# Kernel optimization log

Hardware: AMD Instinct MI355X
Metric: run time of the kernel (lower is better)

Reference implementation:

```python
import jax, jax.numpy as jnp
import numpy as np

N = 10000        # nodes
F_IN = 128       # node features (data.num_node_features)
OUT = 16         # out_channels
H = 32           # attention heads
C1 = 4 * OUT     # hidden per-head dim (4*out_channels)
E = 80000        # directed edges
EPS = 1e-5       # BatchNorm eps
NEG = 0.2        # GATConv LeakyReLU negative_slope


def _gat(x, src, dst, W, a_s, a_d, b, n, C):
    # PyG GATConv, shared lin, concat=False (mean over heads)
    h = (x @ W).reshape(n, H, C)                    # [n,H,C]
    e_src = jnp.sum(h * a_s, -1)                    # [n,H] (alpha from x_j)
    e_dst = jnp.sum(h * a_d, -1)                    # [n,H] (alpha from x_i)
    e = jax.nn.leaky_relu(e_src[src] + e_dst[dst], NEG)     # [E',H]
    m = jax.ops.segment_max(e, dst, num_segments=n)         # segment softmax
    p = jnp.exp(e - m[dst])
    z = jax.ops.segment_sum(p, dst, num_segments=n)
    alpha = p / z[dst]
    out = jax.ops.segment_sum(alpha[:, :, None] * h[src], dst, num_segments=n)
    return out.mean(1) + b                          # mean over heads + bias


def _bn(x, g, b, m, v):  # eval-mode BatchNorm1d (running stats)
    return (x - m) * g / jnp.sqrt(v + EPS) + b


def setup_inputs():
    k = jax.random.split(jax.random.key(0), 40)
    rn = lambda i, s, sc=0.1: jax.random.normal(k[i], s, jnp.float32) * sc
    d = {"x": jax.random.normal(k[0], (N, F_IN), jnp.float32),
         "edge_index": jax.random.randint(k[1], (2, E), 0, N, jnp.int32)}
    # 4 GATConv layers
    d.update(W1=rn(2, (F_IN, H * C1)), as1=rn(3, (H, C1)), ad1=rn(4, (H, C1)), b1=rn(5, (C1,)))
    d.update(W2=rn(6, (C1, H * OUT)), as2=rn(7, (H, OUT)), ad2=rn(8, (H, OUT)), b2=rn(9, (OUT,)))
    d.update(W3=rn(10, (F_IN, H * C1)), as3=rn(11, (H, C1)), ad3=rn(12, (H, C1)), b3=rn(13, (C1,)))
    d.update(W4=rn(14, (C1, H * OUT)), as4=rn(15, (H, OUT)), ad4=rn(16, (H, OUT)), b4=rn(17, (OUT,)))
    # ResidualNetwork(1 block): 1x1 Conv1d over L=1 == matmul
    d.update(rwa=rn(18, (F_IN, OUT)), rba=rn(19, (OUT,)),
             bn1g=jnp.ones(OUT), bn1b=jnp.zeros(OUT), bn1m=rn(20, (OUT,)), bn1v=jnp.abs(rn(21, (OUT,))) + 1.0,
             rwb=rn(22, (OUT, OUT)), rbb=rn(23, (OUT,)),
             bn2g=jnp.ones(OUT), bn2b=jnp.zeros(OUT), bn2m=rn(24, (OUT,)), bn2v=jnp.abs(rn(25, (OUT,))) + 1.0,
             wsc=rn(26, (F_IN, OUT)), bsc=rn(27, (OUT,)),
             bnsg=jnp.ones(OUT), bnsb=jnp.zeros(OUT), bnsm=rn(28, (OUT,)), bnsv=jnp.abs(rn(29, (OUT,))) + 1.0,
             wfc=rn(30, (OUT, OUT)), bfc=rn(31, (OUT,)))
    return d


def reference(x, edge_index, W1, as1, ad1, b1, W2, as2, ad2, b2,
              W3, as3, ad3, b3, W4, as4, ad4, b4,
              rwa, rba, bn1g, bn1b, bn1m, bn1v, rwb, rbb, bn2g, bn2b, bn2m, bn2v,
              wsc, bsc, bnsg, bnsb, bnsm, bnsv, wfc, bfc):
    n = x.shape[0]
    loops = jnp.arange(n, dtype=edge_index.dtype)  # add_self_loops=True
    s2t_src = jnp.concatenate([edge_index[0], loops])  # flow source_to_target
    s2t_dst = jnp.concatenate([edge_index[1], loops])
    t2s_src = jnp.concatenate([edge_index[1], loops])  # flow target_to_source
    t2s_dst = jnp.concatenate([edge_index[0], loops])
    # dropout in original is unassigned (no-op); eval mode assumed
    x_s = jax.nn.elu(_gat(x, s2t_src, s2t_dst, W1, as1, ad1, b1, n, C1))
    x_in = jax.nn.elu(_gat(x_s, s2t_src, s2t_dst, W2, as2, ad2, b2, n, OUT))
    x_t = jax.nn.elu(_gat(x, t2s_src, t2s_dst, W3, as3, ad3, b3, n, C1))
    x_out = jax.nn.elu(_gat(x_t, t2s_src, t2s_dst, W4, as4, ad4, b4, n, OUT))
    # ResidualNetwork: block + identity avg-pool (L=1) + fc
    h = jax.nn.relu(_bn(x @ rwa + rba, bn1g, bn1b, bn1m, bn1v))
    h = _bn(h @ rwb + rbb, bn2g, bn2b, bn2m, bn2v)
    sc = _bn(x @ wsc + bsc, bnsg, bnsb, bnsm, bnsv)
    x_self = jax.nn.relu(h + sc) @ wfc + bfc
    return (x_in, x_out, x_self)
```

## Files before the change

### kernel.cpp

```cpp
#include <hip/hip_runtime.h>
#include <stdint.h>

__device__ __forceinline__ float bf2f(unsigned short u) {
  union { unsigned int i; float f; } v; v.i = ((unsigned int)u) << 16; return v.f;
}
__device__ __forceinline__ unsigned short f2bf(float f) {
  union { float f; unsigned int i; } v; v.f = f;
  unsigned int i = v.i;
  unsigned int r = (i + 0x7fffu + ((i >> 16) & 1u)) >> 16;
  return (unsigned short)r;
}

typedef __bf16 bf16x8 __attribute__((ext_vector_type(8)));
typedef float f32x4 __attribute__((ext_vector_type(4)));
typedef float f32x2 __attribute__((ext_vector_type(2)));
union ABfrag { int4 i4; bf16x8 v; };

#if __has_builtin(__builtin_amdgcn_cvt_pk_fp8_f32) && __has_builtin(__builtin_amdgcn_cvt_pk_f32_fp8)
#define HW_FP8 1
#else
#define HW_FP8 0
#endif

__device__ __forceinline__ unsigned char f2fp8_sw(float f) {
  union { float f; unsigned int u; } v; v.f = f;
  unsigned int s = (v.u >> 24) & 0x80;
  float a = fabsf(f);
  if (a >= 448.f) return (unsigned char)(s | 0x7E);
  v.f = a;
  int ex = (int)(v.u >> 23);
  unsigned int man = v.u & 0x7FFFFFu;
  if (ex >= 121) {
    unsigned int val = ((unsigned int)(ex - 120) << 3) | (man >> 20);
    unsigned int rem = man & 0xFFFFFu;
    if (rem > 0x80000u || (rem == 0x80000u && (val & 1))) val++;
    if (val > 0x7E) val = 0x7E;
    return (unsigned char)(s | val);
  }
  int q = (int)(a * 512.f + 0.5f);
  if (q > 8) q = 8;
  return (unsigned char)(s | (unsigned int)q);
}
__device__ __forceinline__ float fp8dec_sw(unsigned char c) {
  unsigned int e = (c >> 3) & 15u, m = c & 7u;
  float v;
  if (e) { union { unsigned int u; float f; } x; x.u = ((e + 120) << 23) | (m << 20); v = x.f; }
  else v = (float)m * 0.001953125f;
  return (c & 0x80) ? -v : v;
}
__device__ __forceinline__ unsigned char f2fp8(float f) {
#if HW_FP8
  int v = __builtin_amdgcn_cvt_pk_fp8_f32(f, f, 0, false);
  return (unsigned char)(v & 0xFF);
#else
  return f2fp8_sw(f);
#endif
}
__device__ __forceinline__ void dec16p(int4 g, f32x2 o[8]) {
#if HW_FP8
  o[0] = __builtin_amdgcn_cvt_pk_f32_fp8(g.x, false);
  o[1] = __builtin_amdgcn_cvt_pk_f32_fp8(g.x, true);
  o[2] = __builtin_amdgcn_cvt_pk_f32_fp8(g.y, false);
  o[3] = __builtin_amdgcn_cvt_pk_f32_fp8(g.y, true);
  o[4] = __builtin_amdgcn_cvt_pk_f32_fp8(g.z, false);
  o[5] = __builtin_amdgcn_cvt_pk_f32_fp8(g.z, true);
  o[6] = __builtin_amdgcn_cvt_pk_f32_fp8(g.w, false);
  o[7] = __builtin_amdgcn_cvt_pk_f32_fp8(g.w, true);
#else
  unsigned int w[4] = {(unsigned)g.x, (unsigned)g.y, (unsigned)g.z, (unsigned)g.w};
#pragma unroll
  for (int d = 0; d < 4; ++d) {
    unsigned int x = w[d];
    o[d * 2 + 0] = (f32x2){fp8dec_sw((unsigned char)(x & 0xFF)),
                           fp8dec_sw((unsigned char)((x >> 8) & 0xFF))};
    o[d * 2 + 1] = (f32x2){fp8dec_sw((unsigned char)((x >> 16) & 0xFF)),
                           fp8dec_sw((unsigned char)((x >> 24) & 0xFF))};
  }
#endif
}

__device__ __forceinline__ float lrelu_clamp(float e) {
  e = (e > 0.f) ? e : 0.2f * e;
  return fminf(e, 80.f);
}

__global__ __launch_bounds__(256) void k_detect(const unsigned int* __restrict__ x, int* flag,
                                                int* __restrict__ degAB, int ndeg2) {
  if (blockIdx.x == 0) {
    __shared__ int cnt;
    if (threadIdx.x == 0) cnt = 0;
    __syncthreads();
    int c = 0;
    for (int i = threadIdx.x; i < 1024; i += 256) {
      unsigned int lo = x[i] & 0xFFFFu;
      int ex = (int)((lo >> 7) & 0xFF);
      if (ex >= 100 && ex <= 140) c++;
    }
    atomicAdd(&cnt, c);
    __syncthreads();
    if (threadIdx.x == 0) flag[0] = (cnt > 600) ? 1 : 0;
    return;
  }
  for (int idx = (blockIdx.x - 1) * 256 + threadIdx.x; idx < ndeg2; idx += 8 * 256) degAB[idx] = 0;
}

struct PrepDesc {
  const void* csrc[32]; float* cdst[32]; int cn[32];
  const void* x; float* xc; unsigned short* xp;
  const void* W1; const void* W2; const void* W3; const void* W4;
  unsigned short* P1; unsigned short* P2; unsigned short* P3; unsigned short* P4;
  int* degAB;
  const int* ei;
  int nxb, xtotal, ctotal, E, nn;
};
__global__ __launch_bounds__(256) void k_prep(PrepDesc d, const int* __restrict__ flag) {
  int isbf = *flag;
  int b = blockIdx.x;
  if (b < d.nxb) {
    int i = b * 256 + threadIdx.x;
    if (i < d.xtotal) {
      float v = isbf ? bf2f(((const unsigned short*)d.x)[i]) : ((const float*)d.x)[i];
      d.xc[i] = v;
      int row = i >> 7, c = i & 127;
      int tm = row >> 4, mr = row & 15;
      int s = c >> 5, quad = (c >> 3) & 3, j = c & 7;
      size_t idx = (((size_t)tm * 4 + s) * 64 + quad * 16 + mr) * 8 + j;
      d.xp[idx] = f2bf(v);
    }
    return;
  }
  b -= d.nxb;
  if (b < 288) {
    int u = b * 256 + threadIdx.x;
    const void* W; unsigned short* P; int K, N, lu;
    if (u < 32768)      { W = d.W1; P = d.P1; K = 128; N = 2048; lu = u; }
    else if (u < 36864) { W = d.W2; P = d.P2; K = 64;  N = 512;  lu = u - 32768; }
    else if (u < 69632) { W = d.W3; P = d.P3; K = 128; N = 2048; lu = u - 36864; }
    else                { W = d.W4; P = d.P4; K = 64;  N = 512;  lu = u - 69632; }
    int ksteps = K >> 5;
    int g = lu / (ksteps * 64);
    int rem = lu - g * (ksteps * 64);
    int s = rem >> 6, lane = rem & 63;
    int mr = lane & 15, quad = lane >> 4;
    int col = g * 16 + mr;
    int kbase = s * 32 + quad * 8;
#pragma unroll
    for (int j = 0; j < 8; ++j) {
      size_t src = (size_t)(kbase + j) * N + col;
      float v = isbf ? bf2f(((const unsigned short*)W)[src]) : ((const float*)W)[src];
      P[(size_t)lu * 8 + j] = f2bf(v);
    }
    return;
  }
  b -= 288;
  if (b < 4) {
    for (int idx = b * 256 + threadIdx.x; idx < d.ctotal; idx += 4 * 256) {
      int t = 0, off = idx;
      while (off >= d.cn[t]) { off -= d.cn[t]; ++t; }
      float v = isbf ? bf2f(((const unsigned short*)d.csrc[t])[off])
                     : ((const float*)d.csrc[t])[off];
      d.cdst[t][off] = v;
    }
    return;
  }
  b -= 4;
  {
    int e = b * 256 + threadIdx.x;
    if (e < d.E) {
      atomicAdd(&d.degAB[d.ei[d.E + e]], 1);
      atomicAdd(&d.degAB[d.nn + d.ei[e]], 1);
    }
  }
}

__global__ __launch_bounds__(1024) void k_exscan2(const int* __restrict__ degA, const int* __restrict__ degB,
                                                  int* __restrict__ rowA, int* __restrict__ rowB,
                                                  int* __restrict__ colA, int* __restrict__ colB,
                                                  int* __restrict__ curA, int* __restrict__ curB, int n) {
  const int* deg = (blockIdx.x == 0) ? degA : degB;
  int* row = (blockIdx.x == 0) ? rowA : rowB;
  int* colx = (blockIdx.x == 0) ? colA : colB;
  int* curx = (blockIdx.x == 0) ? curA : curB;
  __shared__ int wsum[16], wbase[16];
  __shared__ int carry;
  if (threadIdx.x == 0) carry = 0;
  __syncthreads();
  int lane = threadIdx.x & 63, w = threadIdx.x >> 6;
  int chunks = (n + 1023) >> 10;
  for (int ch = 0; ch < chunks; ++ch) {
    int i = (ch << 10) + threadIdx.x;
    int v = (i < n) ? deg[i] : 0;
    int sc = v;
#pragma unroll
    for (int o = 1; o < 64; o <<= 1) { int t = __shfl_up(sc, o); if (lane >= o) sc += t; }
    if (lane == 63) wsum[w] = sc;
    __syncthreads();
    if (threadIdx.x < 16) {
      int v2 = wsum[threadIdx.x], s2 = v2;
#pragma unroll
      for (int o = 1; o < 16; o <<= 1) { int t = __shfl_up(s2, o); if (lane >= o) s2 += t; }
      wbase[threadIdx.x] = s2 - v2;
      if (threadIdx.x == 15) wsum[15] = s2;
    }
    __syncthreads();
    if (i < n) {
      int rv = carry + wbase[w] + (sc - v) + i;
      row[i] = rv;
      colx[rv] = i;
      curx[i] = rv + 1;
    }
    __syncthreads();
    if (threadIdx.x == 0) carry += wsum[15];
    __syncthreads();
  }
  if (threadIdx.x == 0) row[n] = carry + n;
}

union SMem {
  unsigned char tile[4][16][64];
  struct { float xs[16][128]; float ha[16][16]; float tt[16][16]; } res;
};

template<int CH, int KSTEPS>
__device__ __forceinline__ void mm_es_body(int vblk,
    const unsigned short* __restrict__ Ap, const unsigned short* __restrict__ Bp,
    unsigned char* __restrict__ C, const float* __restrict__ a_s, const float* __restrict__ a_d,
    float* __restrict__ es, float* __restrict__ ed, int N, SMem* sm) {
  int wid = threadIdx.x >> 6;
  int wg = vblk * 4 + wid;
  int ntiles = N >> 6;
  int tm = wg / ntiles, tn = wg % ntiles;
  int lane = threadIdx.x & 63;
  int mr = lane & 15, quad = lane >> 4;
  const unsigned short* ap = Ap + ((size_t)tm * KSTEPS) * 512 + lane * 8;
  const unsigned short* bp = Bp + ((size_t)tn * 4 * KSTEPS) * 512 + lane * 8;
  f32x4 acc[4];
#pragma unroll
  for (int i = 0; i < 4; i++) acc[i] = (f32x4){0.f, 0.f, 0.f, 0.f};
#pragma unroll
  for (int s = 0; s < KSTEPS; ++s) {
    ABfrag a; a.i4 = *(const int4*)(ap + s * 512);
#pragma unroll
    for (int nt = 0; nt < 4; ++nt) {
      ABfrag b; b.i4 = *(const int4*)(bp + (size_t)(nt * KSTEPS + s) * 512);
      acc[nt] = __builtin_amdgcn_mfma_f32_16x16x32_bf16(a.v, b.v, acc[nt], 0, 0, 0);
    }
  }
#pragma unroll
  for (int nt = 0; nt < 4; ++nt)
#pragma unroll
    for (int r = 0; r < 4; ++r)
      sm->tile[wid][quad * 4 + r][nt * 16 + mr] = f2fp8(acc[nt][r]);
  __syncthreads();
  {
    int r16 = lane >> 2, seg = lane & 3;
    int4 val = *(const int4*)&sm->tile[wid][r16][seg * 16];
    *(int4*)(C + (size_t)(tm * 16 + r16) * N + tn * 64 + seg * 16) = val;
  }
  if (CH == 64) {
    float pes[4] = {0.f,0.f,0.f,0.f}, ped[4] = {0.f,0.f,0.f,0.f};
    const float* asr = a_s + tn * 64;
    const float* adr = a_d + tn * 64;
#pragma unroll
    for (int nt = 0; nt < 4; ++nt) {
      float ws = asr[nt * 16 + mr], wd = adr[nt * 16 + mr];
#pragma unroll
      for (int r = 0; r < 4; ++r) { pes[r] += acc[nt][r] * ws; ped[r] += acc[nt][r] * wd; }
    }
#pragma unroll
    for (int m = 1; m < 16; m <<= 1)
#pragma unroll
      for (int r = 0; r < 4; ++r) {
        pes[r] += __shfl_xor(pes[r], m);
        ped[r] += __shfl_xor(ped[r], m);
      }
    if (mr == 0) {
#pragma unroll
      for (int r = 0; r < 4; ++r) {
        int row = tm * 16 + quad * 4 + r;
        es[row * 32 + tn] = pes[r];
        ed[row * 32 + tn] = ped[r];
      }
    }
  } else {
    float pes[4][4], ped[4][4];
#pragma unroll
    for (int nt = 0; nt < 4; ++nt) {
      float ws = a_s[(tn * 4 + nt) * 16 + mr];
      float wd = a_d[(tn * 4 + nt) * 16 + mr];
#pragma unroll
      for (int r = 0; r < 4; ++r) { pes[nt][r] = acc[nt][r] * ws; ped[nt][r] = acc[nt][r] * wd; }
    }
#pragma unroll
    for (int m = 1; m < 16; m <<= 1)
#pragma unroll
      for (int nt = 0; nt < 4; ++nt)
#pragma unroll
        for (int r = 0; r < 4; ++r) {
          pes[nt][r] += __shfl_xor(pes[nt][r], m);
          ped[nt][r] += __shfl_xor(ped[nt][r], m);
        }
    if (mr == 0) {
#pragma unroll
      for (int nt = 0; nt < 4; ++nt)
#pragma unroll
        for (int r = 0; r < 4; ++r) {
          int row = tm * 16 + quad * 4 + r;
          es[row * 32 + tn * 4 + nt] = pes[nt][r];
          ed[row * 32 + tn * 4 + nt] = ped[nt][r];
        }
    }
  }
}

struct MM13Desc {
  const unsigned short* Ap;
  const unsigned short* B1; const unsigned short* B3;
  unsigned char* C1; unsigned char* C3;
  const float* as1; const float* ad1; const float* as3; const float* ad3;
  float* es1; float* ed1; float* es3; float* ed3;
  int sblks, mmblks, resblks, E;
  const int* ei; int* colA; int* colB; int* curA; int* curB;
  const float* xc;
  const float* rp[20];
  void* outbase; size_t eoff; int n;
  const int* flag;
};
__global__ __launch_bounds__(256) void k_mm13res(MM13Desc d) {
  __shared__ SMem sm;
  int b = blockIdx.x;
  if (b < d.sblks) {
    int e = b * 256 + threadIdx.x;
    if (e < d.E) {
      int s = d.ei[e], dd = d.ei[d.E + e];
      d.colA[atomicAdd(&d.curA[dd], 1)] = s;
      d.colB[atomicAdd(&d.curB[s], 1)] = dd;
    }
    return;
  }
  b -= d.sblks;
  if (b < d.mmblks) {
    mm_es_body<64,4>(b, d.Ap, d.B1, d.C1, d.as1, d.ad1, d.es1, d.ed1, 2048, &sm);
    return;
  }
  b -= d.mmblks;
  if (b < d.mmblks) {
    mm_es_body<64,4>(b, d.Ap, d.B3, d.C3, d.as3, d.ad3, d.es3, d.ed3, 2048, &sm);
    return;
  }
  b -= d.mmblks;
  int nodebase = b * 16;
  for (int t = threadIdx.x; t < 16 * 128; t += 256)
    sm.res.xs[t >> 7][t & 127] = d.xc[(size_t)(nodebase + (t >> 7)) * 128 + (t & 127)];
  __syncthreads();
  int ni = threadIdx.x >> 4, c = threadIdx.x & 15;
  const float* rwa = d.rp[0]; const float* rba = d.rp[1];
  const float* bn1g = d.rp[2]; const float* bn1b = d.rp[3];
  const float* bn1m = d.rp[4]; const float* bn1v = d.rp[5];
  const float* rwb = d.rp[6]; const float* rbb = d.rp[7];
  const float* bn2g = d.rp[8]; const float* bn2b = d.rp[9];
  const float* bn2m = d.rp[10]; const float* bn2v = d.rp[11];
  const float* wsc = d.rp[12]; const float* bsc = d.rp[13];
  const float* bnsg = d.rp[14]; const float* bnsb = d.rp[15];
  const float* bnsm = d.rp[16]; const float* bnsv = d.rp[17];
  const float* wfc = d.rp[18]; const float* bfc = d.rp[19];
  float ya = 0.f, ysc = 0.f;
  for (int k = 0; k < 128; ++k) {
    float xv = sm.res.xs[ni][k];
    ya  += xv * rwa[k * 16 + c];
    ysc += xv * wsc[k * 16 + c];
  }
  ya += rba[c]; ysc += bsc[c];
  float s1 = bn1g[c] * rsqrtf(bn1v[c] + 1e-5f);
  ya = (ya - bn1m[c]) * s1 + bn1b[c];
  ya = fmaxf(ya, 0.f);
  float ss = bnsg[c] * rsqrtf(bnsv[c] + 1e-5f);
  ysc = (ysc - bnsm[c]) * ss + bnsb[c];
  sm.res.ha[ni][c] = ya;
  __syncthreads();
  float h2 = rbb[c];
  for (int k = 0; k < 16; ++k) h2 += sm.res.ha[ni][k] * rwb[k * 16 + c];
  float s2 = bn2g[c] * rsqrtf(bn2v[c] + 1e-5f);
  h2 = (h2 - bn2m[c]) * s2 + bn2b[c];
  sm.res.tt[ni][c] = fmaxf(h2 + ysc, 0.f);
  __syncthreads();
  float o = bfc[c];
  for (int k = 0; k < 16; ++k) o += sm.res.tt[ni][k] * wfc[k * 16 + c];
  size_t oo = d.eoff + (size_t)(nodebase + ni) * 16 + c;
  if (*d.flag) ((unsigned short*)d.outbase)[oo] = f2bf(o);
  else         ((float*)d.outbase)[oo] = o;
}

__global__ __launch_bounds__(256) void k_g64(const unsigned char* __restrict__ h1,
                                             const unsigned char* __restrict__ h3,
                                             const float* __restrict__ es1, const float* __restrict__ ed1,
                                             const float* __restrict__ es3, const float* __restrict__ ed3,
                                             const int* __restrict__ rowA, const int* __restrict__ colA,
                                             const int* __restrict__ rowB, const int* __restrict__ colB,
                                             const float* __restrict__ b1, const float* __restrict__ b3,
                                             unsigned short* __restrict__ xsp, unsigned short* __restrict__ xtp,
                                             int n, int gb) {
  int b = blockIdx.x;
  const unsigned char* h; const float *es, *ed, *bias; const int *rowp, *col; unsigned short* outp;
  if (b < gb) { h = h1; es = es1; ed = ed1; rowp = rowA; col = colA; bias = b1; outp = xsp; }
  else { b -= gb; h = h3; es = es3; ed = ed3; rowp = rowB; col = colB; bias = b3; outp = xtp; }
  int wid = threadIdx.x >> 6, lane = threadIdx.x & 63;
  int i = b * 4 + wid;
  if (i >= n) return;
  int hd0 = lane >> 2, hd1 = 16 + hd0;
  float e0 = ed[i * 32 + hd0];
  float e1 = ed[i * 32 + hd1];
  int beg = rowp[i], end = rowp[i + 1];
  int deg = end - beg;
  int colv = (lane < deg) ? col[beg + lane] : 0;
  f32x2 acc0[8], acc1[8];
#pragma unroll
  for (int k = 0; k < 8; ++k) { acc0[k] = (f32x2){0.f, 0.f}; acc1[k] = (f32x2){0.f, 0.f}; }
  float Z0 = 0.f, Z1 = 0.f;
  int s0 = __shfl(colv, 0);
  const int4* hp0 = (const int4*)(h + (size_t)s0 * 2048);
  int4 ng0 = hp0[lane];
  int4 ng1 = hp0[64 + lane];
  float na = es[s0 * 32 + hd0];
  float nb = es[s0 * 32 + hd1];
  for (int j = 0; j < deg; ++j) {
    int4 g0 = ng0, g1 = ng1;
    float ea = na, eb = nb;
    int jn = j + 1;
    if (jn < deg) {
      int sn = (jn < 64) ? __shfl(colv, jn) : col[beg + jn];
      const int4* hq = (const int4*)(h + (size_t)sn * 2048);
      ng0 = hq[lane];
      ng1 = hq[64 + lane];
      na = es[sn * 32 + hd0];
      nb = es[sn * 32 + hd1];
    }
    float q0 = __expf(lrelu_clamp(ea + e0));
    float q1 = __expf(lrelu_clamp(eb + e1));
    Z0 += q0; Z1 += q1;
    f32x2 d0[8], d1[8];
    dec16p(g0, d0); dec16p(g1, d1);
    f32x2 q0v = (f32x2){q0, q0}, q1v = (f32x2){q1, q1};
#pragma unroll
    for (int k = 0; k < 8; ++k) {
      acc0[k] = __builtin_elementwise_fma(q0v, d0[k], acc0[k]);
      acc1[k] = __builtin_elementwise_fma(q1v, d1[k], acc1[k]);
    }
  }
  float zi0 = 1.0f / Z0, zi1 = 1.0f / Z1;
  f32x2 zi0v = (f32x2){zi0, zi0}, zi1v = (f32x2){zi1, zi1};
  f32x2 v2[8];
#pragma unroll
  for (int k = 0; k < 8; ++k)
    v2[k] = __builtin_elementwise_fma(acc1[k], zi1v, acc0[k] * zi0v);
#pragma unroll
  for (int m = 4; m < 64; m <<= 1)
#pragma unroll
    for (int k = 0; k < 8; ++k) {
      v2[k].x += __shfl_xor(v2[k].x, m);
      v2[k].y += __shfl_xor(v2[k].y, m);
    }
  if (lane < 4) {
    float v[16];
#pragma unroll
    for (int k = 0; k < 8; ++k) { v[2 * k] = v2[k].x; v[2 * k + 1] = v2[k].y; }
    int tm = i >> 4, mr = i & 15;
    unsigned short ob[16];
#pragma unroll
    for (int k = 0; k < 16; ++k) {
      float t = v[k] * (1.f / 32.f) + bias[lane * 16 + k];
      t = (t > 0.f) ? t : (__expf(t) - 1.f);
      ob[k] = f2bf(t);
    }
    int s0w = lane >> 1;
#pragma unroll
    for (int g2 = 0; g2 < 2; ++g2) {
      size_t idx = (((size_t)tm * 2 + s0w) * 64 + ((lane & 1) * 2 + g2) * 16 + mr) * 8;
      *(int4*)(outp + idx) = *(const int4*)(ob + g2 * 8);
    }
  }
}

__global__ __launch_bounds__(256) void k_mm24(const unsigned short* __restrict__ xsp,
                                              const unsigned short* __restrict__ xtp,
                                              const unsigned short* __restrict__ W2p,
                                              const unsigned short* __restrict__ W4p,
                                              unsigned char* __restrict__ h2, unsigned char* __restrict__ h4,
                                              const float* __restrict__ as2, const float* __restrict__ ad2,
                                              const float* __restrict__ as4, const float* __restrict__ ad4,
                                              float* __restrict__ es2, float* __restrict__ ed2,
                                              float* __restrict__ es4, float* __restrict__ ed4,
                                              int mmblks) {
  __shared__ SMem sm;
  int b = blockIdx.x;
  if (b < mmblks)
    mm_es_body<16,2>(b, xsp, W2p, h2, as2, ad2, es2, ed2, 512, &sm);
  else
    mm_es_body<16,2>(b - mmblks, xtp, W4p, h4, as4, ad4, es4, ed4, 512, &sm);
}

__global__ __launch_bounds__(256) void k_g16(const unsigned char* __restrict__ h2,
                                             const unsigned char* __restrict__ h4,
                                             const float* __restrict__ es2, const float* __restrict__ ed2,
                                             const float* __restrict__ es4, const float* __restrict__ ed4,
                                             const int* __restrict__ rowA, const int* __restrict__ colA,
                                             const int* __restrict__ rowB, const int* __restrict__ colB,
                                             const float* __restrict__ b2, const float* __restrict__ b4,
                                             void* __restrict__ outbase, int n, int gb,
                                             const int* __restrict__ flag) {
  int b = blockIdx.x;
  const unsigned char* h; const float *es, *ed, *bias; const int *rowp, *col; size_t eoff;
  if (b < gb) { h = h2; es = es2; ed = ed2; rowp = rowA; col = colA; bias = b2; eoff = 0; }
  else { b -= gb; h = h4; es = es4; ed = ed4; rowp = rowB; col = colB; bias = b4; eoff = (size_t)n * 16; }
  int wid = threadIdx.x >> 6, lane = threadIdx.x & 63;
  int i = b * 4 + wid;
  if (i >= n) return;
  int hh = lane & 31, j2 = lane >> 5;
  float ev = ed[i * 32 + hh];
  int beg = rowp[i], end = rowp[i + 1];
  int deg = end - beg;
  int colv = (lane < deg) ? col[beg + lane] : 0;
  f32x2 acc[8];
#pragma unroll
  for (int k = 0; k < 8; ++k) acc[k] = (f32x2){0.f, 0.f};
  float Z = 0.f;
  int j = j2;
  int4 ng = (int4){0, 0, 0, 0};
  float ne = 0.f;
  if (j < deg) {
    int s = __shfl(colv, j);
    ng = ((const int4*)(h + (size_t)s * 512))[hh];
    ne = es[s * 32 + hh];
  }
  for (; j < deg; j += 2) {
    int4 g = ng; float ee = ne;
    int jn = j + 2;
    if (jn < deg) {
      int sn = (jn < 64) ? __shfl(colv, jn) : col[beg + jn];
      ng = ((const int4*)(h + (size_t)sn * 512))[hh];
      ne = es[sn * 32 + hh];
    }
    float q = __expf(lrelu_clamp(ee + ev));
    Z += q;
    f32x2 d[8];
    dec16p(g, d);
    f32x2 qv = (f32x2){q, q};
#pragma unroll
    for (int k = 0; k < 8; ++k) acc[k] = __builtin_elementwise_fma(qv, d[k], acc[k]);
  }
  Z += __shfl_xor(Z, 32);
  float zi = 1.0f / Z;
  f32x2 ziv = (f32x2){zi, zi};
  f32x2 v2[8];
#pragma unroll
  for (int k = 0; k < 8; ++k) v2[k] = acc[k] * ziv;
#pragma unroll
  for (int m = 1; m < 64; m <<= 1)
#pragma unroll
    for (int k = 0; k < 8; ++k) {
      v2[k].x += __shfl_xor(v2[k].x, m);
      v2[k].y += __shfl_xor(v2[k].y, m);
    }
  if (lane == 0) {
    float v[16];
#pragma unroll
    for (int k = 0; k < 8; ++k) { v[2 * k] = v2[k].x; v[2 * k + 1] = v2[k].y; }
    int isbf = *flag;
    if (isbf) {
      unsigned short ob[16];
#pragma unroll
      for (int k = 0; k < 16; ++k) {
        float t = v[k] * (1.f / 32.f) + bias[k];
        t = (t > 0.f) ? t : (__expf(t) - 1.f);
        ob[k] = f2bf(t);
      }
      unsigned short* o = (unsigned short*)outbase + eoff + (size_t)i * 16;
      *(int4*)o = *(const int4*)ob;
      *(int4*)(o + 8) = *(const int4*)(ob + 8);
    } else {
      float* o = (float*)outbase + eoff + (size_t)i * 16;
#pragma unroll
      for (int k = 0; k < 16; ++k) {
        float t = v[k] * (1.f / 32.f) + bias[k];
        t = (t > 0.f) ? t : (__expf(t) - 1.f);
        o[k] = t;
      }
    }
  }
}

extern "C" void kernel_launch(void* const* d_in, const int* in_sizes, int n_in,
                              void* d_out, int out_size, void* d_ws, size_t ws_size,
                              hipStream_t stream) {
  const int n = in_sizes[0] / 128;
  const int E = in_sizes[1] / 2;
  const int* ei = (const int*)d_in[1];

  char* wsp = (char*)d_ws; size_t off = 0;
  auto alloc = [&](size_t bytes) -> void* {
    void* p = wsp + off; off = (off + bytes + 255) & ~(size_t)255; return p;
  };
  int* flag = (int*)alloc(4);
  float* xc = (float*)alloc((size_t)n * 128 * 4);
  unsigned short* xp = (unsigned short*)alloc((size_t)n * 128 * 2);
  unsigned short* W1p = (unsigned short*)alloc((size_t)2048 * 128 * 2);
  unsigned short* W2p = (unsigned short*)alloc((size_t)512 * 64 * 2);
  unsigned short* W3p = (unsigned short*)alloc((size_t)2048 * 128 * 2);
  unsigned short* W4p = (unsigned short*)alloc((size_t)512 * 64 * 2);
  unsigned char* h1 = (unsigned char*)alloc((size_t)n * 2048);
  unsigned char* h3 = (unsigned char*)alloc((size_t)n * 2048);
  unsigned char* h2 = (unsigned char*)alloc((size_t)n * 512);
  unsigned char* h4 = (unsigned char*)alloc((size_t)n * 512);
  float* es1 = (float*)alloc((size_t)n * 32 * 4);
  float* ed1 = (float*)alloc((size_t)n * 32 * 4);
  float* es3 = (float*)alloc((size_t)n * 32 * 4);
  float* ed3 = (float*)alloc((size_t)n * 32 * 4);
  float* es2 = (float*)alloc((size_t)n * 32 * 4);
  float* ed2 = (float*)alloc((size_t)n * 32 * 4);
  float* es4 = (float*)alloc((size_t)n * 32 * 4);
  float* ed4 = (float*)alloc((size_t)n * 32 * 4);
  unsigned short* xsp = (unsigned short*)alloc((size_t)n * 64 * 2);
  unsigned short* xtp = (unsigned short*)alloc((size_t)n * 64 * 2);
  int* rowA = (int*)alloc((size_t)(n + 1) * 4);
  int* rowB = (int*)alloc((size_t)(n + 1) * 4);
  int* colA = (int*)alloc((size_t)(E + n) * 4);
  int* colB = (int*)alloc((size_t)(E + n) * 4);
  int* degAB = (int*)alloc((size_t)2 * n * 4);
  int* degA = degAB, * degB = degAB + n;
  int* curA = (int*)alloc((size_t)n * 4);
  int* curB = (int*)alloc((size_t)n * 4);

  static const int cidx[32] = {3,4,5, 7,8,9, 11,12,13, 15,16,17,
                               18,19,20,21,22,23,24,25,26,27,28,29,
                               30,31,32,33,34,35,36,37};
  PrepDesc pd;
  float* canon[38] = {nullptr};
  pd.ctotal = 0;
  for (int t = 0; t < 32; ++t) {
    int ii = cidx[t];
    canon[ii] = (float*)alloc((size_t)in_sizes[ii] * 4);
    pd.csrc[t] = d_in[ii];
    pd.cdst[t] = canon[ii];
    pd.cn[t] = in_sizes[ii];
    pd.ctotal += in_sizes[ii];
  }
  pd.x = d_in[0]; pd.xc = xc; pd.xp = xp;
  pd.W1 = d_in[2]; pd.W2 = d_in[6]; pd.W3 = d_in[10]; pd.W4 = d_in[14];
  pd.P1 = W1p; pd.P2 = W2p; pd.P3 = W3p; pd.P4 = W4p;
  pd.degAB = degAB;
  pd.ei = ei;
  pd.nxb = (n * 128 + 255) / 256;
  pd.xtotal = n * 128;
  pd.E = E;
  pd.nn = n;
  (void)ws_size; (void)n_in; (void)out_size;

  const int degblks = (E + 255) / 256;

  k_detect<<<9, 256, 0, stream>>>((const unsigned int*)d_in[0], flag, degAB, 2 * n);
  k_prep<<<pd.nxb + 288 + 4 + degblks, 256, 0, stream>>>(pd, flag);
  k_exscan2<<<2, 1024, 0, stream>>>(degA, degB, rowA, rowB, colA, colB, curA, curB, n);

  const int mt = n / 16;
  const int mmblks64 = mt * 32 / 4;
  const int mmblks16 = mt * 8 / 4;
  const int gb = (n + 3) / 4;

  MM13Desc md;
  md.Ap = xp; md.B1 = W1p; md.B3 = W3p; md.C1 = h1; md.C3 = h3;
  md.as1 = canon[3]; md.ad1 = canon[4]; md.as3 = canon[11]; md.ad3 = canon[12];
  md.es1 = es1; md.ed1 = ed1; md.es3 = es3; md.ed3 = ed3;
  md.sblks = degblks; md.mmblks = mmblks64; md.resblks = mt; md.E = E;
  md.ei = ei; md.colA = colA; md.colB = colB; md.curA = curA; md.curB = curB;
  md.xc = xc;
  for (int t = 0; t < 20; ++t) md.rp[t] = canon[18 + t];
  md.outbase = d_out; md.eoff = (size_t)2 * n * 16; md.n = n; md.flag = flag;
  k_mm13res<<<degblks + 2 * mmblks64 + mt, 256, 0, stream>>>(md);

  k_g64<<<2 * gb, 256, 0, stream>>>(h1, h3, es1, ed1, es3, ed3,
                                    rowA, colA, rowB, colB,
                                    canon[5], canon[13], xsp, xtp, n, gb);
  k_mm24<<<2 * mmblks16, 256, 0, stream>>>(xsp, xtp, W2p, W4p, h2, h4,
                                           canon[7], canon[8], canon[15], canon[16],
                                           es2, ed2, es4, ed4, mmblks16);
  k_g16<<<2 * gb, 256, 0, stream>>>(h2, h4, es2, ed2, es4, ed4,
                                    rowA, colA, rowB, colB,
                                    canon[9], canon[17], d_out, n, gb, flag);
}
```

Before: 319.9 us.

## Register-block node-feature GEMMs over four row tiles with A staged in LDS

Each block of the GAT projection GEMMs now covers four 16-row tiles. It first stages their A fragments in shared memory, then each wave accumulates a 4x4 grid of MFMA tiles, so every loaded W fragment is reused across four row tiles. This cuts repeated global loads of B and shrinks the grid by roughly four times. The cost is higher accumulator register pressure, an extra LDS staging pass with a barrier, and fewer blocks to spread across the GPU.

```diff
diff --git a/kernel.cpp b/kernel.cpp
--- a/kernel.cpp
+++ b/kernel.cpp
@@ -217,98 +217,129 @@
 }
 
 union SMem {
-  unsigned char tile[4][16][64];
+  struct { int4 a[1024]; unsigned char tile[4][16][64]; } mm;
   struct { float xs[16][128]; float ha[16][16]; float tt[16][16]; } res;
 };
 
 template<int CH, int KSTEPS>
-__device__ __forceinline__ void mm_es_body(int vblk,
+__device__ __forceinline__ void mm_es64_body(int rg, int cg, int MT,
     const unsigned short* __restrict__ Ap, const unsigned short* __restrict__ Bp,
     unsigned char* __restrict__ C, const float* __restrict__ a_s, const float* __restrict__ a_d,
     float* __restrict__ es, float* __restrict__ ed, int N, SMem* sm) {
+  const int TI = KSTEPS * 64;
+  int vt = MT - rg * 4; if (vt > 4) vt = 4;
+  {
+    const int4* src = (const int4*)(Ap + (size_t)rg * 4 * TI * 8);
+    int tot = vt * TI;
+    for (int t = threadIdx.x; t < tot; t += 256) sm->mm.a[t] = src[t];
+  }
+  __syncthreads();
   int wid = threadIdx.x >> 6;
-  int wg = vblk * 4 + wid;
-  int ntiles = N >> 6;
-  int tm = wg / ntiles, tn = wg % ntiles;
+  int tn = cg * 4 + wid;
   int lane = threadIdx.x & 63;
   int mr = lane & 15, quad = lane >> 4;
-  const unsigned short* ap = Ap + ((size_t)tm * KSTEPS) * 512 + lane * 8;
   const unsigned short* bp = Bp + ((size_t)tn * 4 * KSTEPS) * 512 + lane * 8;
-  f32x4 acc[4];
-#pragma unroll
-  for (int i = 0; i < 4; i++) acc[i] = (f32x4){0.f, 0.f, 0.f, 0.f};
+  f32x4 acc[4][4];
+#pragma unroll
+  for (int rt = 0; rt < 4; ++rt)
+#pragma unroll
+    for (int nt = 0; nt < 4; ++nt) acc[rt][nt] = (f32x4){0.f, 0.f, 0.f, 0.f};
 #pragma unroll
   for (int s = 0; s < KSTEPS; ++s) {
-    ABfrag a; a.i4 = *(const int4*)(ap + s * 512);
-#pragma unroll
-    for (int nt = 0; nt < 4; ++nt) {
-      ABfrag b; b.i4 = *(const int4*)(bp + (size_t)(nt * KSTEPS + s) * 512);
-      acc[nt] = __builtin_amdgcn_mfma_f32_16x16x32_bf16(a.v, b.v, acc[nt], 0, 0, 0);
-    }
-  }
-#pragma unroll
-  for (int nt = 0; nt < 4; ++nt)
-#pragma unroll
-    for (int r = 0; r < 4; ++r)
-      sm->tile[wid][quad * 4 + r][nt * 16 + mr] = f2fp8(acc[nt][r]);
-  __syncthreads();
-  {
-    int r16 = lane >> 2, seg = lane & 3;
-    int4 val = *(const int4*)&sm->tile[wid][r16][seg * 16];
-    *(int4*)(C + (size_t)(tm * 16 + r16) * N + tn * 64 + seg * 16) = val;
+    ABfrag bfr[4];
+#pragma unroll
+    for (int nt = 0; nt < 4; ++nt) bfr[nt].i4 = *(const int4*)(bp + (size_t)(nt * KSTEPS + s) * 512);
+    ABfrag afr[4];
+#pragma unroll
+    for (int rt = 0; rt < 4; ++rt) afr[rt].i4 = sm->mm.a[rt * TI + s * 64 + lane];
+#pragma unroll
+    for (int nt = 0; nt < 4; ++nt)
+#pragma unroll
+      for (int rt = 0; rt < 4; ++rt)
+        acc[rt][nt] = __builtin_amdgcn_mfma_f32_16x16x32_bf16(afr[rt].v, bfr[nt].v, acc[rt][nt], 0, 0, 0);
+  }
+  int r16 = lane >> 2, seg = lane & 3;
+#pragma unroll
+  for (int rt = 0; rt < 4; ++rt) {
+    if (rt < vt) {
+      int tm = rg * 4 + rt;
+#pragma unroll
+      for (int nt = 0; nt < 4; ++nt)
+#pragma unroll
+        for (int r = 0; r < 4; ++r)
+          sm->mm.tile[wid][quad * 4 + r][nt * 16 + mr] = f2fp8(acc[rt][nt][r]);
+      int4 val = *(const int4*)&sm->mm.tile[wid][r16][seg * 16];
+      *(int4*)(C + (size_t)(tm * 16 + r16) * N + tn * 64 + seg * 16) = val;
+    }
   }
   if (CH == 64) {
-    float pes[4] = {0.f,0.f,0.f,0.f}, ped[4] = {0.f,0.f,0.f,0.f};
     const float* asr = a_s + tn * 64;
     const float* adr = a_d + tn * 64;
+    float ws[4], wd[4];
+#pragma unroll
+    for (int nt = 0; nt < 4; ++nt) { ws[nt] = asr[nt * 16 + mr]; wd[nt] = adr[nt * 16 + mr]; }
+#pragma unroll
+    for (int rt = 0; rt < 4; ++rt) {
+      if (rt < vt) {
+        int tm = rg * 4 + rt;
+        float pes[4] = {0.f,0.f,0.f,0.f}, ped[4] = {0.f,0.f,0.f,0.f};
+#pragma unroll
+        for (int nt = 0; nt < 4; ++nt)
+#pragma unroll
+          for (int r = 0; r < 4; ++r) { pes[r] += acc[rt][nt][r] * ws[nt]; ped[r] += acc[rt][nt][r] * wd[nt]; }
+#pragma unroll
+        for (int m = 1; m < 16; m <<= 1)
+#pragma unroll
+          for (int r = 0; r < 4; ++r) {
+            pes[r] += __shfl_xor(pes[r], m);
+            ped[r] += __shfl_xor(ped[r], m);
+          }
+        if (mr == 0) {
+#pragma unroll
+          for (int r = 0; r < 4; ++r) {
+            int row = tm * 16 + quad * 4 + r;
+            es[row * 32 + tn] = pes[r];
+            ed[row * 32 + tn] = ped[r];
+          }
+        }
+      }
+    }
+  } else {
+    float ws[4], wd[4];
 #pragma unroll
     for (int nt = 0; nt < 4; ++nt) {
-      float ws = asr[nt * 16 + mr], wd = adr[nt * 16 + mr];
-#pragma unroll
-      for (int r = 0; r < 4; ++r) { pes[r] += acc[nt][r] * ws; ped[r] += acc[nt][r] * wd; }
-    }
-#pragma unroll
-    for (int m = 1; m < 16; m <<= 1)
-#pragma unroll
-      for (int r = 0; r < 4; ++r) {
-        pes[r] += __shfl_xor(pes[r], m);
-        ped[r] += __shfl_xor(ped[r], m);
+      ws[nt] = a_s[(tn * 4 + nt) * 16 + mr];
+      wd[nt] = a_d[(tn * 4 + nt) * 16 + mr];
+    }
+#pragma unroll
+    for (int rt = 0; rt < 4; ++rt) {
+      if (rt < vt) {
+        int tm = rg * 4 + rt;
+        float pes[4][4], ped[4][4];
+#pragma unroll
+        for (int nt = 0; nt < 4; ++nt)
+#pragma unroll
+          for (int r = 0; r < 4; ++r) { pes[nt][r] = acc[rt][nt][r] * ws[nt]; ped[nt][r] = acc[rt][nt][r] * wd[nt]; }
+#pragma unroll
+        for (int m = 1; m < 16; m <<= 1)
+#pragma unroll
+          for (int nt = 0; nt < 4; ++nt)
+#pragma unroll
+            for (int r = 0; r < 4; ++r) {
+              pes[nt][r] += __shfl_xor(pes[nt][r], m);
+              ped[nt][r] += __shfl_xor(ped[nt][r], m);
+            }
+        if (mr == 0) {
+#pragma unroll
+          for (int nt = 0; nt < 4; ++nt)
+#pragma unroll
+            for (int r = 0; r < 4; ++r) {
+              int row = tm * 16 + quad * 4 + r;
+              es[row * 32 + tn * 4 + nt] = pes[nt][r];
+              ed[row * 32 + tn * 4 + nt] = ped[nt][r];
+            }
+        }
       }
-    if (mr == 0) {
-#pragma unroll
-      for (int r = 0; r < 4; ++r) {
-        int row = tm * 16 + quad * 4 + r;
-        es[row * 32 + tn] = pes[r];
-        ed[row * 32 + tn] = ped[r];
-      }
-    }
-  } else {
-    float pes[4][4], ped[4][4];
-#pragma unroll
-    for (int nt = 0; nt < 4; ++nt) {
-      float ws = a_s[(tn * 4 + nt) * 16 + mr];
-      float wd = a_d[(tn * 4 + nt) * 16 + mr];
-#pragma unroll
-      for (int r = 0; r < 4; ++r) { pes[nt][r] = acc[nt][r] * ws; ped[nt][r] = acc[nt][r] * wd; }
-    }
-#pragma unroll
-    for (int m = 1; m < 16; m <<= 1)
-#pragma unroll
-      for (int nt = 0; nt < 4; ++nt)
-#pragma unroll
-        for (int r = 0; r < 4; ++r) {
-          pes[nt][r] += __shfl_xor(pes[nt][r], m);
-          ped[nt][r] += __shfl_xor(ped[nt][r], m);
-        }
-    if (mr == 0) {
-#pragma unroll
-      for (int nt = 0; nt < 4; ++nt)
-#pragma unroll
-        for (int r = 0; r < 4; ++r) {
-          int row = tm * 16 + quad * 4 + r;
-          es[row * 32 + tn * 4 + nt] = pes[nt][r];
-          ed[row * 32 + tn * 4 + nt] = ped[nt][r];
-        }
     }
   }
 }
@@ -319,7 +350,7 @@
   unsigned char* C1; unsigned char* C3;
   const float* as1; const float* ad1; const float* as3; const float* ad3;
   float* es1; float* ed1; float* es3; float* ed3;
-  int sblks, mmblks, resblks, E;
+  int sblks, mmblks, E, mt;
   const int* ei; int* colA; int* colB; int* curA; int* curB;
   const float* xc;
   const float* rp[20];
@@ -340,12 +371,12 @@
   }
   b -= d.sblks;
   if (b < d.mmblks) {
-    mm_es_body<64,4>(b, d.Ap, d.B1, d.C1, d.as1, d.ad1, d.es1, d.ed1, 2048, &sm);
+    mm_es64_body<64,4>(b >> 3, b & 7, d.mt, d.Ap, d.B1, d.C1, d.as1, d.ad1, d.es1, d.ed1, 2048, &sm);
     return;
   }
   b -= d.mmblks;
   if (b < d.mmblks) {
-    mm_es_body<64,4>(b, d.Ap, d.B3, d.C3, d.as3, d.ad3, d.es3, d.ed3, 2048, &sm);
+    mm_es64_body<64,4>(b >> 3, b & 7, d.mt, d.Ap, d.B3, d.C3, d.as3, d.ad3, d.es3, d.ed3, 2048, &sm);
     return;
   }
   b -= d.mmblks;
@@ -490,13 +521,15 @@
                                               const float* __restrict__ as4, const float* __restrict__ ad4,
                                               float* __restrict__ es2, float* __restrict__ ed2,
                                               float* __restrict__ es4, float* __restrict__ ed4,
-                                              int mmblks) {
+                                              int mmblks, int mt) {
   __shared__ SMem sm;
   int b = blockIdx.x;
   if (b < mmblks)
-    mm_es_body<16,2>(b, xsp, W2p, h2, as2, ad2, es2, ed2, 512, &sm);
-  else
-    mm_es_body<16,2>(b - mmblks, xtp, W4p, h4, as4, ad4, es4, ed4, 512, &sm);
+    mm_es64_body<16,2>(b >> 1, b & 1, mt, xsp, W2p, h2, as2, ad2, es2, ed2, 512, &sm);
+  else {
+    b -= mmblks;
+    mm_es64_body<16,2>(b >> 1, b & 1, mt, xtp, W4p, h4, as4, ad4, es4, ed4, 512, &sm);
+  }
 }
 
 __global__ __launch_bounds__(256) void k_g16(const unsigned char* __restrict__ h2,
@@ -662,15 +695,16 @@
   k_exscan2<<<2, 1024, 0, stream>>>(degA, degB, rowA, rowB, colA, colB, curA, curB, n);
 
   const int mt = n / 16;
-  const int mmblks64 = mt * 32 / 4;
-  const int mmblks16 = mt * 8 / 4;
+  const int nrg = (mt + 3) / 4;
+  const int mmblks64 = nrg * 8;
+  const int mmblks16 = nrg * 2;
   const int gb = (n + 3) / 4;
 
   MM13Desc md;
   md.Ap = xp; md.B1 = W1p; md.B3 = W3p; md.C1 = h1; md.C3 = h3;
   md.as1 = canon[3]; md.ad1 = canon[4]; md.as3 = canon[11]; md.ad3 = canon[12];
   md.es1 = es1; md.ed1 = ed1; md.es3 = es3; md.ed3 = ed3;
-  md.sblks = degblks; md.mmblks = mmblks64; md.resblks = mt; md.E = E;
+  md.sblks = degblks; md.mmblks = mmblks64; md.E = E; md.mt = mt;
   md.ei = ei; md.colA = colA; md.colB = colB; md.curA = curA; md.curB = curB;
   md.xc = xc;
   for (int t = 0; t < 20; ++t) md.rp[t] = canon[18 + t];
@@ -682,7 +716,7 @@
                                     canon[5], canon[13], xsp, xtp, n, gb);
   k_mm24<<<2 * mmblks16, 256, 0, stream>>>(xsp, xtp, W2p, W4p, h2, h4,
                                            canon[7], canon[8], canon[15], canon[16],
-                                           es2, ed2, es4, ed4, mmblks16);
+                                           es2, ed2, es4, ed4, mmblks16, mt);
   k_g16<<<2 * gb, 256, 0, stream>>>(h2, h4, es2, ed2, es4, ed4,
                                     rowA, colA, rowB, colB,
                                     canon[9], canon[17], d_out, n, gb, flag);
```

Result: slower. 327.6 us (+2.4%).
